# Kernel optimization log

Measured on AMD Instinct MI355X. Metric: run time of the kernel, lower is better.

## Reference

```python
import jax, jax.numpy as jnp
import numpy as np

HID, NH, QLR, KVLR, QK, VH, RH = 7168, 128, 1536, 512, 128, 128, 64
EPS = 1.1920929e-07  # torch.finfo(float32).eps, RMSNorm eps=None default
ROPE_BASE = 10000.0


def _rmsnorm(x, w):
    return x * jax.lax.rsqrt(jnp.mean(x * x, axis=-1, keepdims=True) + EPS) * w


def _rope_tables(seq_len, dim):
    inv_freq = 1.0 / (ROPE_BASE ** (np.arange(0, dim, 2, dtype=np.float32) / dim))
    t = np.arange(seq_len, dtype=np.float32)
    freqs = np.outer(t, inv_freq)          # [S, dim/2]
    emb = np.concatenate([freqs, freqs], -1)  # [S, dim]
    return jnp.asarray(np.cos(emb)), jnp.asarray(np.sin(emb))


def _apply_rope(x, cos, sin):
    # x: [B, H, S, D]; rotate-half convention matching the torch module
    d = x.shape[-1]
    x1, x2 = x[..., : d // 2], x[..., d // 2 :]
    rotated = jnp.concatenate([-x2, x1], axis=-1)
    return x * cos + rotated * sin


def setup_inputs() -> dict:
    key = jax.random.key(0)
    ks = jax.random.split(key, 9)
    def w(k, out_dim, in_dim):
        return jax.random.normal(k, (out_dim, in_dim), jnp.float32) / np.sqrt(in_dim)
    return {
        "hidden_states": jax.random.normal(ks[0], (1, 1024, HID), jnp.float32),
        "w_q_down": w(ks[1], QLR, HID),
        "q_norm_w": jnp.ones((QLR,), jnp.float32),
        "w_q_up": w(ks[2], NH * (QK + RH), QLR),
        "w_kv_down": w(ks[3], KVLR + RH, HID),
        "kv_norm_w": jnp.ones((KVLR,), jnp.float32),
        "w_kv_up": w(ks[4], NH * (QK + VH), KVLR),
        "w_out": w(ks[5], HID, NH * VH),
    }


def reference(hidden_states, w_q_down, q_norm_w, w_q_up, w_kv_down, kv_norm_w, w_kv_up, w_out):
    B, S, _ = hidden_states.shape
    cos, sin = _rope_tables(S, RH)

    # Q path: down -> RMSNorm -> up, split into non-rope / rope parts
    c_q = jnp.einsum("bsh,qh->bsq", hidden_states, w_q_down)            # [B,S,QLR]
    q_cr = jnp.einsum("bsq,oq->bso", _rmsnorm(c_q, q_norm_w), w_q_up)   # [B,S,NH*(QK+RH)]
    q_cr = q_cr.reshape(B, S, NH, QK + RH).transpose(0, 2, 1, 3)        # [B,NH,S,QK+RH]
    q_c, q_r = q_cr[..., :QK], q_cr[..., QK:]

    # KV path: shared latent + MQA rope key
    ckv_kr = jnp.einsum("bsh,oh->bso", hidden_states, w_kv_down)        # [B,S,KVLR+RH]
    c_kv, k_r = ckv_kr[..., :KVLR], ckv_kr[..., KVLR:]
    k_r = k_r[:, None, :, :]                                            # [B,1,S,RH]
    kv = jnp.einsum("bsq,oq->bso", _rmsnorm(c_kv, kv_norm_w), w_kv_up)  # [B,S,NH*(QK+VH)]
    kv = kv.reshape(B, S, NH, QK + VH).transpose(0, 2, 1, 3)            # [B,NH,S,QK+VH]
    k_c, v = kv[..., :QK], kv[..., QK:]

    q_r = _apply_rope(q_r, cos, sin)
    k_r = _apply_rope(k_r, cos, sin)

    q = jnp.concatenate([q_c, q_r], axis=-1)                            # [B,NH,S,QK+RH]
    k = jnp.concatenate([k_c, jnp.broadcast_to(k_r, (B, NH, S, RH))], axis=-1)

    scale = 1.0 / np.sqrt(QK + RH)
    scores = jnp.einsum("bhqd,bhkd->bhqk", q, k) * scale
    attn = jax.nn.softmax(scores, axis=-1)
    o = jnp.einsum("bhqk,bhkd->bhqd", attn, v)                          # [B,NH,S,VH]
    o = o.transpose(0, 2, 1, 3).reshape(B, S, NH * VH)
    return jnp.einsum("bso,ho->bsh", o, w_out)
```

## Files before the change

### kernel.cpp

```cpp
#include <hip/hip_runtime.h>
#include <hip/hip_bf16.h>
#include <math.h>

#define HIDN 7168
#define NHEAD 128
#define QLRANK 1536
#define KVLRANK 512
#define QKD 128
#define VHD 128
#define RHD 64
#define SEQ 1024
#define RMS_EPS 1.1920929e-07f

typedef unsigned short u16;
typedef __attribute__((ext_vector_type(8))) short bf16x8;
typedef __attribute__((ext_vector_type(4))) float f32x4;
typedef __attribute__((ext_vector_type(8))) unsigned short u16x8;

__device__ __forceinline__ u16 f2bf(float f) {
    unsigned int u = __float_as_uint(f);
    unsigned int r = (u + 0x7FFFu + ((u >> 16) & 1u)) >> 16;
    return (u16)r;
}
__device__ __forceinline__ float bf2f(u16 v) {
    return __uint_as_float(((unsigned int)v) << 16);
}

__device__ __forceinline__ void gld_lds16(const u16* g, u16* l) {
    __builtin_amdgcn_global_load_lds(
        (const __attribute__((address_space(1))) unsigned int*)g,
        (__attribute__((address_space(3))) unsigned int*)l,
        16, 0, 0);
}

__global__ __launch_bounds__(256) void conv3(const float* __restrict__ s0, u16* __restrict__ d0, long n0,
                                             const float* __restrict__ s1, u16* __restrict__ d1, long n1,
                                             const float* __restrict__ s2, u16* __restrict__ d2, long n2) {
    const long stride = (long)gridDim.x * blockDim.x * 8;
#pragma unroll 1
    for (int seg = 0; seg < 3; ++seg) {
        const float* s = seg == 0 ? s0 : (seg == 1 ? s1 : s2);
        u16* d        = seg == 0 ? d0 : (seg == 1 ? d1 : d2);
        long n        = seg == 0 ? n0 : (seg == 1 ? n1 : n2);
        for (long i = ((long)blockIdx.x * blockDim.x + threadIdx.x) * 8; i < n; i += stride) {
            float4 a = *(const float4*)(s + i);
            float4 b = *(const float4*)(s + i + 4);
            u16x8 o;
            o[0] = f2bf(a.x); o[1] = f2bf(a.y); o[2] = f2bf(a.z); o[3] = f2bf(a.w);
            o[4] = f2bf(b.x); o[5] = f2bf(b.y); o[6] = f2bf(b.z); o[7] = f2bf(b.w);
            *(u16x8*)(d + i) = o;
        }
    }
}

__global__ __launch_bounds__(256) void f32_to_bf16(const float* __restrict__ in,
                                                   u16* __restrict__ out, long n) {
    long i = ((long)blockIdx.x * blockDim.x + threadIdx.x) * 8;
    long stride = (long)gridDim.x * blockDim.x * 8;
    for (; i < n; i += stride) {
        float4 a = *(const float4*)(in + i);
        float4 b = *(const float4*)(in + i + 4);
        u16x8 o;
        o[0] = f2bf(a.x); o[1] = f2bf(a.y); o[2] = f2bf(a.z); o[3] = f2bf(a.w);
        o[4] = f2bf(b.x); o[5] = f2bf(b.y); o[6] = f2bf(b.z); o[7] = f2bf(b.w);
        *(u16x8*)(out + i) = o;
    }
}

template <int OUT_BF16, int FCONV>
__global__ __launch_bounds__(512) void gemm_bt(const u16* __restrict__ A,
                                               const u16* __restrict__ B,
                                               void* __restrict__ Cv,
                                               int M, int N, int Kslice, long ldk,
                                               const float* __restrict__ cvsrc,
                                               u16* __restrict__ cvdst,
                                               long cvtotal) {
    __shared__ u16 As[2 * 128 * 64];
    __shared__ u16 Bs[2 * 128 * 64];
    const int tid = threadIdx.x;
    const int lane = tid & 63;
    const int w = tid >> 6;
    const int wr = w >> 2, wc = w & 3;
    const int l15 = lane & 15, lg = lane >> 4;
    const int n0 = blockIdx.x * 128;
    const int m0 = blockIdx.y * 128;
    const long kbase = (long)blockIdx.z * Kslice;

    const u16* asrc[2];
    const u16* bsrc[2];
    int aoff[2];
#pragma unroll
    for (int i = 0; i < 2; ++i) {
        int r = (w * 2 + i) * 8 + (lane >> 3);
        int gc = (lane & 7) ^ (r & 7);
        asrc[i] = A + (long)(m0 + r) * ldk + kbase + gc * 8;
        int br = n0 + r; if (br >= N) br = N - 1;
        bsrc[i] = B + (long)br * ldk + kbase + gc * 8;
        aoff[i] = (w * 2 + i) * 512;
    }

    long gbase = 0, gend = 0;
    int nwin = 0;
    float4 cva, cvb;
    long gprev = -1;
    if (FCONV) {
        const int nblocks = gridDim.x * gridDim.y * gridDim.z;
        const int bl = (blockIdx.z * gridDim.y + blockIdx.y) * gridDim.x + blockIdx.x;
        long share = (cvtotal + nblocks - 1) / nblocks;
        gbase = (long)bl * share;
        gend = gbase + share; if (gend > cvtotal) gend = cvtotal;
        nwin = (int)((share + 511) >> 9);
    }

    f32x4 acc[4][2];
    const f32x4 z = {0.f, 0.f, 0.f, 0.f};
#pragma unroll
    for (int i = 0; i < 4; ++i)
#pragma unroll
        for (int j = 0; j < 2; ++j) acc[i][j] = z;

    auto stage = [&](int bufi, int kofs) {
#pragma unroll
        for (int i = 0; i < 2; ++i) {
            gld_lds16(asrc[i] + kofs, As + bufi * 8192 + aoff[i]);
            gld_lds16(bsrc[i] + kofs, Bs + bufi * 8192 + aoff[i]);
        }
    };

    const int nsteps = Kslice >> 6;
    stage(0, 0);
    asm volatile("s_waitcnt vmcnt(0)" ::: "memory");
    __builtin_amdgcn_s_barrier();

    int cur = 0;
    for (int t = 0; t < nsteps; ++t) {
        if (t + 1 < nsteps) stage(cur ^ 1, (t + 1) * 64);
        if (FCONV) {
            if (gprev >= 0) {
                u16x8 o;
                o[0] = f2bf(cva.x); o[1] = f2bf(cva.y); o[2] = f2bf(cva.z); o[3] = f2bf(cva.w);
                o[4] = f2bf(cvb.x); o[5] = f2bf(cvb.y); o[6] = f2bf(cvb.z); o[7] = f2bf(cvb.w);
                *(u16x8*)(cvdst + gprev * 8) = o;
            }
            gprev = -1;
            if (t < nwin) {
                long g = gbase + (long)t * 512 + tid;
                if (g < gend) {
                    cva = *(const float4*)(cvsrc + g * 8);
                    cvb = *(const float4*)(cvsrc + g * 8 + 4);
                    gprev = g;
                }
            }
        }
        const u16* Ab = As + cur * 8192;
        const u16* Bb = Bs + cur * 8192;
#pragma unroll
        for (int kk = 0; kk < 2; ++kk) {
            bf16x8 a[4], b[2];
#pragma unroll
            for (int i = 0; i < 4; ++i) {
                int row = wr * 64 + i * 16 + l15;
                a[i] = *(const bf16x8*)&Ab[row * 64 + ((kk * 4 + lg) ^ (row & 7)) * 8];
            }
#pragma unroll
            for (int j = 0; j < 2; ++j) {
                int row = wc * 32 + j * 16 + l15;
                b[j] = *(const bf16x8*)&Bb[row * 64 + ((kk * 4 + lg) ^ (row & 7)) * 8];
            }
#pragma unroll
            for (int i = 0; i < 4; ++i)
#pragma unroll
                for (int j = 0; j < 2; ++j)
                    acc[i][j] = __builtin_amdgcn_mfma_f32_16x16x32_bf16(a[i], b[j], acc[i][j], 0, 0, 0);
        }
        asm volatile("s_waitcnt vmcnt(0)" ::: "memory");
        __builtin_amdgcn_s_barrier();
        cur ^= 1;
    }
    if (FCONV && gprev >= 0) {
        u16x8 o;
        o[0] = f2bf(cva.x); o[1] = f2bf(cva.y); o[2] = f2bf(cva.z); o[3] = f2bf(cva.w);
        o[4] = f2bf(cvb.x); o[5] = f2bf(cvb.y); o[6] = f2bf(cvb.z); o[7] = f2bf(cvb.w);
        *(u16x8*)(cvdst + gprev * 8) = o;
    }

#pragma unroll
    for (int i = 0; i < 4; ++i)
#pragma unroll
        for (int j = 0; j < 2; ++j)
#pragma unroll
            for (int r = 0; r < 4; ++r) {
                int m = m0 + wr * 64 + i * 16 + lg * 4 + r;
                int n = n0 + wc * 32 + j * 16 + l15;
                if (n < N) {
                    if (OUT_BF16)
                        ((u16*)Cv)[(long)m * N + n] = f2bf(acc[i][j][r]);
                    else
                        ((float*)Cv)[(long)blockIdx.z * M * N + (long)m * N + n] = acc[i][j][r];
                }
            }
}

__global__ __launch_bounds__(256) void reduce_rms_cq(const float* __restrict__ parts,
                                                     const float* __restrict__ wnorm,
                                                     u16* __restrict__ y) {
    const int row = blockIdx.x;
    const long mn = (long)SEQ * QLRANK;
    const float* base = parts + (long)row * QLRANK;
    float v[6];
    float ss = 0.f;
#pragma unroll
    for (int i = 0; i < 6; ++i) {
        int col = i * 256 + threadIdx.x;
        float s = base[col];
#pragma unroll
        for (int p = 1; p < 4; ++p) s += base[(long)p * mn + col];
        v[i] = s;
        ss += s * s;
    }
#pragma unroll
    for (int off = 32; off > 0; off >>= 1) ss += __shfl_down(ss, off);
    __shared__ float partial[4];
    if ((threadIdx.x & 63) == 0) partial[threadIdx.x >> 6] = ss;
    __syncthreads();
    float tot = partial[0] + partial[1] + partial[2] + partial[3];
    float rs = 1.0f / sqrtf(tot / (float)QLRANK + RMS_EPS);
    u16* yr = y + (long)row * QLRANK;
#pragma unroll
    for (int i = 0; i < 6; ++i) {
        int col = i * 256 + threadIdx.x;
        yr[col] = f2bf(v[i] * rs * wnorm[col]);
    }
}

__global__ __launch_bounds__(256) void reduce_rms_rope_kv(const float* __restrict__ parts,
                                                          const float* __restrict__ wnorm,
                                                          u16* __restrict__ y,
                                                          const float* __restrict__ cos_t,
                                                          const float* __restrict__ sin_t,
                                                          u16* __restrict__ kr) {
    const int row = blockIdx.x;
    const long mn = (long)SEQ * 576;
    const float* base = parts + (long)row * 576;
    __shared__ float rope_buf[64];
    __shared__ float partial[4];
    float v[3];
    float ss = 0.f;
#pragma unroll
    for (int i = 0; i < 3; ++i) {
        int col = i * 256 + threadIdx.x;
        if (col < 576) {
            float s = base[col];
#pragma unroll
            for (int p = 1; p < 8; ++p) s += base[(long)p * mn + col];
            v[i] = s;
            if (col < KVLRANK) ss += s * s;
            else rope_buf[col - KVLRANK] = s;
        }
    }
#pragma unroll
    for (int off = 32; off > 0; off >>= 1) ss += __shfl_down(ss, off);
    if ((threadIdx.x & 63) == 0) partial[threadIdx.x >> 6] = ss;
    __syncthreads();
    float tot = partial[0] + partial[1] + partial[2] + partial[3];
    float rs = 1.0f / sqrtf(tot / (float)KVLRANK + RMS_EPS);
    u16* yr = y + (long)row * KVLRANK;
#pragma unroll
    for (int i = 0; i < 3; ++i) {
        int col = i * 256 + threadIdx.x;
        if (col < KVLRANK) yr[col] = f2bf(v[i] * rs * wnorm[col]);
    }
    if (threadIdx.x < 32) {
        float x1 = rope_buf[threadIdx.x];
        float x2 = rope_buf[threadIdx.x + 32];
        float c = cos_t[row * 32 + threadIdx.x], sn = sin_t[row * 32 + threadIdx.x];
        kr[row * 64 + threadIdx.x]      = f2bf(x1 * c - x2 * sn);
        kr[row * 64 + threadIdx.x + 32] = f2bf(x2 * c + x1 * sn);
    }
}

__global__ void rope_tables(float* __restrict__ cos_t, float* __restrict__ sin_t) {
    int s = blockIdx.x;
    int i = threadIdx.x;
    float invf = powf(10000.0f, -((float)(2 * i) / 64.0f));
    float ang = (float)s * invf;
    cos_t[s * 32 + i] = cosf(ang);
    sin_t[s * 32 + i] = sinf(ang);
}

__global__ void rope_q(u16* __restrict__ q_cr, const float* __restrict__ cos_t,
                       const float* __restrict__ sin_t) {
    int s = blockIdx.x;
    int h = blockIdx.y * 2 + (threadIdx.x >> 5);
    int i = threadIdx.x & 31;
    u16* base = q_cr + (s * (NHEAD * 192) + h * 192 + QKD);
    float x1 = bf2f(base[i]);
    float x2 = bf2f(base[i + 32]);
    float c = cos_t[s * 32 + i], sn = sin_t[s * 32 + i];
    base[i]      = f2bf(x1 * c - x2 * sn);
    base[i + 32] = f2bf(x2 * c + x1 * sn);
}

__global__ __launch_bounds__(256) void build_vt(const u16* __restrict__ kv,
                                                u16* __restrict__ vT) {
    __shared__ u16 vtile[64][136];
    const int h = blockIdx.x, sb = blockIdx.y, s0 = sb * 64;
    const int tid = threadIdx.x;
#pragma unroll
    for (int it = 0; it < 4; ++it) {
        int c = it * 256 + tid;
        int row = c >> 4;
        int off8 = (c & 15) * 8;
        *(u16x8*)&vtile[row][off8] =
            *(const u16x8*)&kv[(s0 + row) * 32768 + h * 256 + 128 + off8];
    }
    __syncthreads();
    const int sl = tid & 63;
    const int dvb = tid >> 6;
#pragma unroll
    for (int it = 0; it < 32; ++it) {
        int dv = dvb + it * 4;
        vT[(h * 128 + dv) * 1024 + s0 + sl] = vtile[sl][dv];
    }
}

__global__ __launch_bounds__(512) void mla_attn(const u16* __restrict__ q_cr,
                                                const u16* __restrict__ kv,
                                                const u16* __restrict__ kr,
                                                const u16* __restrict__ vT,
                                                u16* __restrict__ o_g,
                                                const float* __restrict__ wsrc,
                                                u16* __restrict__ wdst,
                                                int do_conv) {
    __shared__ u16 ks[64][200];
    __shared__ u16 vts[128][72];
    __shared__ u16 p_lds[8][16][68];
    const int qb = blockIdx.x, h = blockIdx.y;
    const int s0q = qb * 128;
    const int tid = threadIdx.x, lane = tid & 63, w = tid >> 6;
    const int l15 = lane & 15, lg = lane >> 4;
    const float scale = 0.07216878364870323f;

    bf16x8 qreg[6];
    {
        const int qrow = s0q + w * 16 + l15;
#pragma unroll
        for (int kk = 0; kk < 6; ++kk)
            qreg[kk] = *(const bf16x8*)&q_cr[qrow * (NHEAD * 192) + h * 192 + kk * 32 + lg * 8];
    }

    const int krow0 = tid >> 4,           koff0 = (tid & 15) * 8;
    const int krow1 = (512 + tid) >> 4,   koff1 = ((512 + tid) & 15) * 8;
    const int rrow  = tid >> 3,           roff  = (tid & 7) * 8;
    const int vdv0  = tid >> 3,           voff0 = (tid & 7) * 8;
    const int vdv1  = (512 + tid) >> 3,   voff1 = ((512 + tid) & 7) * 8;
    const u16* kvp = kv + h * 256;
    const u16* vtp = vT + (long)(h * 128) * 1024;

    u16x8 kreg0, kreg1, krreg, vreg0, vreg1;
    auto load_tile = [&](int s0k) {
        kreg0 = *(const u16x8*)&kvp[(long)(s0k + krow0) * 32768 + koff0];
        kreg1 = *(const u16x8*)&kvp[(long)(s0k + krow1) * 32768 + koff1];
        krreg = *(const u16x8*)&kr[(s0k + rrow) * 64 + roff];
        vreg0 = *(const u16x8*)&vtp[(long)vdv0 * 1024 + s0k + voff0];
        vreg1 = *(const u16x8*)&vtp[(long)vdv1 * 1024 + s0k + voff1];
    };

    const long cbase = ((long)(h * 8 + qb)) * 16 * 896;
    float4 cva0, cvb0, cva1, cvb1;
    const int gi0 = tid;
    const int gi1 = 512 + tid;
    auto conv_load = [&](int kt) {
        long g0 = cbase + (long)kt * 896;
        long a0 = (g0 + gi0) * 8;
        cva0 = *(const float4*)(wsrc + a0);
        cvb0 = *(const float4*)(wsrc + a0 + 4);
        if (gi1 < 896) {
            long a1 = (g0 + gi1) * 8;
            cva1 = *(const float4*)(wsrc + a1);
            cvb1 = *(const float4*)(wsrc + a1 + 4);
        }
    };
    auto conv_store = [&](int kt) {
        long g0 = cbase + (long)kt * 896;
        u16x8 o;
        o[0] = f2bf(cva0.x); o[1] = f2bf(cva0.y); o[2] = f2bf(cva0.z); o[3] = f2bf(cva0.w);
        o[4] = f2bf(cvb0.x); o[5] = f2bf(cvb0.y); o[6] = f2bf(cvb0.z); o[7] = f2bf(cvb0.w);
        *(u16x8*)(wdst + (g0 + gi0) * 8) = o;
        if (gi1 < 896) {
            u16x8 o1;
            o1[0] = f2bf(cva1.x); o1[1] = f2bf(cva1.y); o1[2] = f2bf(cva1.z); o1[3] = f2bf(cva1.w);
            o1[4] = f2bf(cvb1.x); o1[5] = f2bf(cvb1.y); o1[6] = f2bf(cvb1.z); o1[7] = f2bf(cvb1.w);
            *(u16x8*)(wdst + (g0 + gi1) * 8) = o1;
        }
    };

    f32x4 o_acc[8];
    const f32x4 z = {0.f, 0.f, 0.f, 0.f};
#pragma unroll
    for (int d = 0; d < 8; ++d) o_acc[d] = z;
    float m_r[4], l_r[4];
#pragma unroll
    for (int r = 0; r < 4; ++r) { m_r[r] = -1e30f; l_r[r] = 0.f; }

    load_tile(0);
    if (do_conv) conv_load(0);

    for (int kt = 0; kt < 16; ++kt) {
        __syncthreads();
        *(u16x8*)&ks[krow0][koff0]      = kreg0;
        *(u16x8*)&ks[krow1][koff1]      = kreg1;
        *(u16x8*)&ks[rrow][128 + roff]  = krreg;
        *(u16x8*)&vts[vdv0][voff0]      = vreg0;
        *(u16x8*)&vts[vdv1][voff1]      = vreg1;
        __syncthreads();
        if (kt + 1 < 16) load_tile((kt + 1) * 64);

        if (do_conv) {
            conv_store(kt);
            if (kt + 1 < 16) conv_load(kt + 1);
        }

        f32x4 sf[4];
#pragma unroll
        for (int j = 0; j < 4; ++j) sf[j] = z;
        __builtin_amdgcn_s_setprio(1);
#pragma unroll
        for (int kk = 0; kk < 6; ++kk) {
            bf16x8 a = qreg[kk];
#pragma unroll
            for (int j = 0; j < 4; ++j) {
                bf16x8 b = *(const bf16x8*)&ks[j * 16 + l15][kk * 32 + lg * 8];
                sf[j] = __builtin_amdgcn_mfma_f32_16x16x32_bf16(a, b, sf[j], 0, 0, 0);
            }
        }
        __builtin_amdgcn_s_setprio(0);

        float p[4][4];
        float alpha[4];
#pragma unroll
        for (int r = 0; r < 4; ++r) {
            float mx = fmaxf(fmaxf(sf[0][r], sf[1][r]), fmaxf(sf[2][r], sf[3][r]));
#pragma unroll
            for (int off = 1; off < 16; off <<= 1) mx = fmaxf(mx, __shfl_xor(mx, off));
            mx *= scale;
            float mnew = fmaxf(m_r[r], mx);
            alpha[r] = __expf(m_r[r] - mnew);
            float rs = 0.f;
#pragma unroll
            for (int j = 0; j < 4; ++j) {
                float pv = __expf(sf[j][r] * scale - mnew);
                p[j][r] = pv;
                rs += pv;
            }
#pragma unroll
            for (int off = 1; off < 16; off <<= 1) rs += __shfl_xor(rs, off);
            l_r[r] = l_r[r] * alpha[r] + rs;
            m_r[r] = mnew;
        }
#pragma unroll
        for (int d = 0; d < 8; ++d)
#pragma unroll
            for (int r = 0; r < 4; ++r) o_acc[d][r] *= alpha[r];

#pragma unroll
        for (int j = 0; j < 4; ++j)
#pragma unroll
            for (int r = 0; r < 4; ++r)
                p_lds[w][lg * 4 + r][j * 16 + l15] = f2bf(p[j][r]);

        __builtin_amdgcn_s_setprio(1);
#pragma unroll
        for (int kk2 = 0; kk2 < 2; ++kk2) {
            bf16x8 a = *(const bf16x8*)&p_lds[w][l15][kk2 * 32 + lg * 8];
#pragma unroll
            for (int d = 0; d < 8; ++d) {
                bf16x8 b = *(const bf16x8*)&vts[d * 16 + l15][kk2 * 32 + lg * 8];
                o_acc[d] = __builtin_amdgcn_mfma_f32_16x16x32_bf16(a, b, o_acc[d], 0, 0, 0);
            }
        }
        __builtin_amdgcn_s_setprio(0);
    }

#pragma unroll
    for (int d = 0; d < 8; ++d)
#pragma unroll
        for (int r = 0; r < 4; ++r) {
            int srow = s0q + w * 16 + lg * 4 + r;
            float v = o_acc[d][r] / l_r[r];
            o_g[srow * 16384 + h * 128 + d * 16 + l15] = f2bf(v);
        }
}

extern "C" void kernel_launch(void* const* d_in, const int* in_sizes, int n_in,
                              void* d_out, int out_size, void* d_ws, size_t ws_size,
                              hipStream_t stream) {
    const float* hs        = (const float*)d_in[0];
    const float* w_q_down  = (const float*)d_in[1];
    const float* q_norm_w  = (const float*)d_in[2];
    const float* w_q_up    = (const float*)d_in[3];
    const float* w_kv_down = (const float*)d_in[4];
    const float* kv_norm_w = (const float*)d_in[5];
    const float* w_kv_up   = (const float*)d_in[6];
    const float* w_out     = (const float*)d_in[7];
    float* out = (float*)d_out;
    char* ws = (char*)d_ws;

    const size_t SZ_KV   = (size_t)SEQ * 32768 * 2;
    const size_t SZ_QCR  = (size_t)SEQ * (NHEAD * 192) * 2;
    const size_t SZ_KR   = (size_t)SEQ * 64 * 2;
    const size_t SZ_TAB  = (size_t)SEQ * 32 * 4;
    const size_t SZ_VT   = (size_t)NHEAD * 128 * 1024 * 2;
    const size_t SZ_OG   = (size_t)SEQ * 16384 * 2;
    const size_t SZ_WOUT = (size_t)HIDN * 16384 * 2;
    const size_t SZ_WQD  = (size_t)QLRANK * HIDN * 2;
    const size_t SZ_WQU  = (size_t)24576 * QLRANK * 2;
    const size_t SZ_WKD  = (size_t)576 * HIDN * 2;
    const size_t SZ_WKU  = (size_t)32768 * KVLRANK * 2;
    const size_t SZ_PART = (size_t)4 * SEQ * QLRANK * 4;
    const size_t SZ_HS   = (size_t)SEQ * HIDN * 2;
    const size_t SZ_CQN  = (size_t)SEQ * QLRANK * 2;
    const size_t SZ_CKVN = (size_t)SEQ * KVLRANK * 2;

    size_t off = 0;
    u16* kvb     = (u16*)(ws + off); off += SZ_KV;
    u16* q_cr    = (u16*)(ws + off); off += SZ_QCR;
    u16* kr      = (u16*)(ws + off); off += SZ_KR;
    float* cos_t = (float*)(ws + off); off += SZ_TAB;
    float* sin_t = (float*)(ws + off); off += SZ_TAB;
    u16* vT      = (u16*)(ws + off); off += SZ_VT;
    u16* o_g     = (u16*)(ws + off); off += SZ_OG;
    const size_t live_end = off;
    u16* wout_bf = (u16*)(ws + live_end);
    size_t toff = live_end;
    u16* wqd_bf  = (u16*)(ws + toff); toff += SZ_WQD;
    u16* wqu_bf  = (u16*)(ws + toff); toff += SZ_WQU;
    u16* wkd_bf  = (u16*)(ws + toff); toff += SZ_WKD;
    u16* wku_bf  = (u16*)(ws + toff); toff += SZ_WKU;
    float* parts = (float*)(ws + toff); toff += SZ_PART;
    u16* hs_bf    = (u16*)(ws + toff); toff += SZ_HS;
    u16* cq_n     = (u16*)(ws + toff); toff += SZ_CQN;
    u16* ckv_n    = (u16*)(ws + toff); toff += SZ_CKVN;
    const int fuse = (live_end + SZ_WOUT) <= ws_size;
    (void)in_sizes; (void)n_in; (void)out_size;

    rope_tables<<<dim3(SEQ), dim3(32), 0, stream>>>(cos_t, sin_t);

    conv3<<<2048, 256, 0, stream>>>(hs, hs_bf, (long)SEQ * HIDN,
                                    w_q_down, wqd_bf, (long)QLRANK * HIDN,
                                    w_kv_down, wkd_bf, (long)576 * HIDN);

    gemm_bt<0, 1><<<dim3(QLRANK / 128, SEQ / 128, 4), 512, 0, stream>>>(
        hs_bf, wqd_bf, parts, SEQ, QLRANK, HIDN / 4, HIDN,
        w_q_up, wqu_bf, ((long)24576 * QLRANK) / 8);
    reduce_rms_cq<<<SEQ, 256, 0, stream>>>(parts, q_norm_w, cq_n);

    gemm_bt<1, 1><<<dim3(24576 / 128, SEQ / 128), 512, 0, stream>>>(
        cq_n, wqu_bf, q_cr, SEQ, 24576, QLRANK, QLRANK,
        w_kv_up, wku_bf, ((long)32768 * KVLRANK) / 8);

    gemm_bt<0, 0><<<dim3(5, SEQ / 128, 8), 512, 0, stream>>>(
        hs_bf, wkd_bf, parts, SEQ, 576, HIDN / 8, HIDN, nullptr, nullptr, 0);
    reduce_rms_rope_kv<<<SEQ, 256, 0, stream>>>(parts, kv_norm_w, ckv_n, cos_t, sin_t, kr);

    gemm_bt<1, 0><<<dim3(32768 / 128, SEQ / 128), 512, 0, stream>>>(
        ckv_n, wku_bf, kvb, SEQ, 32768, KVLRANK, KVLRANK, nullptr, nullptr, 0);

    rope_q<<<dim3(SEQ, NHEAD / 2), 64, 0, stream>>>(q_cr, cos_t, sin_t);
    build_vt<<<dim3(NHEAD, SEQ / 64), 256, 0, stream>>>(kvb, vT);

    if (!fuse)
        f32_to_bf16<<<4096, 256, 0, stream>>>(w_out, wout_bf, (long)HIDN * 16384);
    mla_attn<<<dim3(SEQ / 128, NHEAD), 512, 0, stream>>>(q_cr, kvb, kr, vT, o_g,
                                                         w_out, wout_bf, fuse ? 1 : 0);

    gemm_bt<0, 0><<<dim3(HIDN / 128, SEQ / 128), 512, 0, stream>>>(
        o_g, wout_bf, out, SEQ, HIDN, 16384, 16384, nullptr, nullptr, 0);
}
```

Before: 886.8 us.

## Fuse rope tables, q-rope and kv_down conversion into neighboring kernels

Merges the rope table generation into the conversion kernel and moves conversion of w_kv_down from the front conversion pass into the spare-slot conversion of the first down-projection GEMM. It also applies the Q rope rotation inside the attention kernel on the registers holding Q, which removes the separate rope_q launch and its read-modify-write of q_cr. The aim is fewer launches and less standalone memory traffic. The cost is extra branching in the GEMM conversion path and a few extra table loads per attention block.

```diff
diff --git a/kernel.cpp b/kernel.cpp
--- a/kernel.cpp
+++ b/kernel.cpp
@@ -33,15 +33,22 @@
         16, 0, 0);
 }
 
-__global__ __launch_bounds__(256) void conv3(const float* __restrict__ s0, u16* __restrict__ d0, long n0,
-                                             const float* __restrict__ s1, u16* __restrict__ d1, long n1,
-                                             const float* __restrict__ s2, u16* __restrict__ d2, long n2) {
+__global__ __launch_bounds__(256) void conv2_tab(const float* __restrict__ s0, u16* __restrict__ d0, long n0,
+                                                 const float* __restrict__ s1, u16* __restrict__ d1, long n1,
+                                                 float* __restrict__ cos_t, float* __restrict__ sin_t) {
+    if (blockIdx.x < SEQ && threadIdx.x < 32) {
+        int s = blockIdx.x, i = threadIdx.x;
+        float invf = powf(10000.0f, -((float)(2 * i) / 64.0f));
+        float ang = (float)s * invf;
+        cos_t[s * 32 + i] = cosf(ang);
+        sin_t[s * 32 + i] = sinf(ang);
+    }
     const long stride = (long)gridDim.x * blockDim.x * 8;
 #pragma unroll 1
-    for (int seg = 0; seg < 3; ++seg) {
-        const float* s = seg == 0 ? s0 : (seg == 1 ? s1 : s2);
-        u16* d        = seg == 0 ? d0 : (seg == 1 ? d1 : d2);
-        long n        = seg == 0 ? n0 : (seg == 1 ? n1 : n2);
+    for (int seg = 0; seg < 2; ++seg) {
+        const float* s = seg == 0 ? s0 : s1;
+        u16* d        = seg == 0 ? d0 : d1;
+        long n        = seg == 0 ? n0 : n1;
         for (long i = ((long)blockIdx.x * blockDim.x + threadIdx.x) * 8; i < n; i += stride) {
             float4 a = *(const float4*)(s + i);
             float4 b = *(const float4*)(s + i + 4);
@@ -72,9 +79,10 @@
                                                const u16* __restrict__ B,
                                                void* __restrict__ Cv,
                                                int M, int N, int Kslice, long ldk,
-                                               const float* __restrict__ cvsrc,
-                                               u16* __restrict__ cvdst,
-                                               long cvtotal) {
+                                               const float* __restrict__ cvs1,
+                                               u16* __restrict__ cvd1, long cvt1,
+                                               const float* __restrict__ cvs2,
+                                               u16* __restrict__ cvd2, long cvt2) {
     __shared__ u16 As[2 * 128 * 64];
     __shared__ u16 Bs[2 * 128 * 64];
     const int tid = threadIdx.x;
@@ -106,9 +114,10 @@
     if (FCONV) {
         const int nblocks = gridDim.x * gridDim.y * gridDim.z;
         const int bl = (blockIdx.z * gridDim.y + blockIdx.y) * gridDim.x + blockIdx.x;
-        long share = (cvtotal + nblocks - 1) / nblocks;
+        long total = cvt1 + cvt2;
+        long share = (total + nblocks - 1) / nblocks;
         gbase = (long)bl * share;
-        gend = gbase + share; if (gend > cvtotal) gend = cvtotal;
+        gend = gbase + share; if (gend > total) gend = total;
         nwin = (int)((share + 511) >> 9);
     }
 
@@ -140,14 +149,16 @@
                 u16x8 o;
                 o[0] = f2bf(cva.x); o[1] = f2bf(cva.y); o[2] = f2bf(cva.z); o[3] = f2bf(cva.w);
                 o[4] = f2bf(cvb.x); o[5] = f2bf(cvb.y); o[6] = f2bf(cvb.z); o[7] = f2bf(cvb.w);
-                *(u16x8*)(cvdst + gprev * 8) = o;
+                if (gprev < cvt1) *(u16x8*)(cvd1 + gprev * 8) = o;
+                else              *(u16x8*)(cvd2 + (gprev - cvt1) * 8) = o;
             }
             gprev = -1;
             if (t < nwin) {
                 long g = gbase + (long)t * 512 + tid;
                 if (g < gend) {
-                    cva = *(const float4*)(cvsrc + g * 8);
-                    cvb = *(const float4*)(cvsrc + g * 8 + 4);
+                    const float* src = (g < cvt1) ? (cvs1 + g * 8) : (cvs2 + (g - cvt1) * 8);
+                    cva = *(const float4*)(src);
+                    cvb = *(const float4*)(src + 4);
                     gprev = g;
                 }
             }
@@ -181,7 +192,8 @@
         u16x8 o;
         o[0] = f2bf(cva.x); o[1] = f2bf(cva.y); o[2] = f2bf(cva.z); o[3] = f2bf(cva.w);
         o[4] = f2bf(cvb.x); o[5] = f2bf(cvb.y); o[6] = f2bf(cvb.z); o[7] = f2bf(cvb.w);
-        *(u16x8*)(cvdst + gprev * 8) = o;
+        if (gprev < cvt1) *(u16x8*)(cvd1 + gprev * 8) = o;
+        else              *(u16x8*)(cvd2 + (gprev - cvt1) * 8) = o;
     }
 
 #pragma unroll
@@ -279,28 +291,6 @@
     }
 }
 
-__global__ void rope_tables(float* __restrict__ cos_t, float* __restrict__ sin_t) {
-    int s = blockIdx.x;
-    int i = threadIdx.x;
-    float invf = powf(10000.0f, -((float)(2 * i) / 64.0f));
-    float ang = (float)s * invf;
-    cos_t[s * 32 + i] = cosf(ang);
-    sin_t[s * 32 + i] = sinf(ang);
-}
-
-__global__ void rope_q(u16* __restrict__ q_cr, const float* __restrict__ cos_t,
-                       const float* __restrict__ sin_t) {
-    int s = blockIdx.x;
-    int h = blockIdx.y * 2 + (threadIdx.x >> 5);
-    int i = threadIdx.x & 31;
-    u16* base = q_cr + (s * (NHEAD * 192) + h * 192 + QKD);
-    float x1 = bf2f(base[i]);
-    float x2 = bf2f(base[i + 32]);
-    float c = cos_t[s * 32 + i], sn = sin_t[s * 32 + i];
-    base[i]      = f2bf(x1 * c - x2 * sn);
-    base[i + 32] = f2bf(x2 * c + x1 * sn);
-}
-
 __global__ __launch_bounds__(256) void build_vt(const u16* __restrict__ kv,
                                                 u16* __restrict__ vT) {
     __shared__ u16 vtile[64][136];
@@ -329,6 +319,8 @@
                                                 const u16* __restrict__ kr,
                                                 const u16* __restrict__ vT,
                                                 u16* __restrict__ o_g,
+                                                const float* __restrict__ cos_t,
+                                                const float* __restrict__ sin_t,
                                                 const float* __restrict__ wsrc,
                                                 u16* __restrict__ wdst,
                                                 int do_conv) {
@@ -347,6 +339,15 @@
 #pragma unroll
         for (int kk = 0; kk < 6; ++kk)
             qreg[kk] = *(const bf16x8*)&q_cr[qrow * (NHEAD * 192) + h * 192 + kk * 32 + lg * 8];
+#pragma unroll
+        for (int j = 0; j < 8; ++j) {
+            int i = lg * 8 + j;
+            float c = cos_t[qrow * 32 + i], sn = sin_t[qrow * 32 + i];
+            float x1 = bf2f((u16)qreg[4][j]);
+            float x2 = bf2f((u16)qreg[5][j]);
+            qreg[4][j] = (short)f2bf(x1 * c - x2 * sn);
+            qreg[5][j] = (short)f2bf(x2 * c + x1 * sn);
+        }
     }
 
     const int krow0 = tid >> 4,           koff0 = (tid & 15) * 8;
@@ -544,36 +545,39 @@
     const int fuse = (live_end + SZ_WOUT) <= ws_size;
     (void)in_sizes; (void)n_in; (void)out_size;
 
-    rope_tables<<<dim3(SEQ), dim3(32), 0, stream>>>(cos_t, sin_t);
-
-    conv3<<<2048, 256, 0, stream>>>(hs, hs_bf, (long)SEQ * HIDN,
-                                    w_q_down, wqd_bf, (long)QLRANK * HIDN,
-                                    w_kv_down, wkd_bf, (long)576 * HIDN);
+    conv2_tab<<<2048, 256, 0, stream>>>(hs, hs_bf, (long)SEQ * HIDN,
+                                        w_q_down, wqd_bf, (long)QLRANK * HIDN,
+                                        cos_t, sin_t);
 
     gemm_bt<0, 1><<<dim3(QLRANK / 128, SEQ / 128, 4), 512, 0, stream>>>(
         hs_bf, wqd_bf, parts, SEQ, QLRANK, HIDN / 4, HIDN,
-        w_q_up, wqu_bf, ((long)24576 * QLRANK) / 8);
+        w_q_up, wqu_bf, ((long)24576 * QLRANK) / 8,
+        w_kv_down, wkd_bf, ((long)576 * HIDN) / 8);
     reduce_rms_cq<<<SEQ, 256, 0, stream>>>(parts, q_norm_w, cq_n);
 
     gemm_bt<1, 1><<<dim3(24576 / 128, SEQ / 128), 512, 0, stream>>>(
         cq_n, wqu_bf, q_cr, SEQ, 24576, QLRANK, QLRANK,
-        w_kv_up, wku_bf, ((long)32768 * KVLRANK) / 8);
+        w_kv_up, wku_bf, ((long)32768 * KVLRANK) / 8,
+        nullptr, nullptr, 0);
 
     gemm_bt<0, 0><<<dim3(5, SEQ / 128, 8), 512, 0, stream>>>(
-        hs_bf, wkd_bf, parts, SEQ, 576, HIDN / 8, HIDN, nullptr, nullptr, 0);
+        hs_bf, wkd_bf, parts, SEQ, 576, HIDN / 8, HIDN,
+        nullptr, nullptr, 0, nullptr, nullptr, 0);
     reduce_rms_rope_kv<<<SEQ, 256, 0, stream>>>(parts, kv_norm_w, ckv_n, cos_t, sin_t, kr);
 
     gemm_bt<1, 0><<<dim3(32768 / 128, SEQ / 128), 512, 0, stream>>>(
-        ckv_n, wku_bf, kvb, SEQ, 32768, KVLRANK, KVLRANK, nullptr, nullptr, 0);
-
-    rope_q<<<dim3(SEQ, NHEAD / 2), 64, 0, stream>>>(q_cr, cos_t, sin_t);
+        ckv_n, wku_bf, kvb, SEQ, 32768, KVLRANK, KVLRANK,
+        nullptr, nullptr, 0, nullptr, nullptr, 0);
+
     build_vt<<<dim3(NHEAD, SEQ / 64), 256, 0, stream>>>(kvb, vT);
 
     if (!fuse)
         f32_to_bf16<<<4096, 256, 0, stream>>>(w_out, wout_bf, (long)HIDN * 16384);
     mla_attn<<<dim3(SEQ / 128, NHEAD), 512, 0, stream>>>(q_cr, kvb, kr, vT, o_g,
+                                                         cos_t, sin_t,
                                                          w_out, wout_bf, fuse ? 1 : 0);
 
     gemm_bt<0, 0><<<dim3(HIDN / 128, SEQ / 128), 512, 0, stream>>>(
-        o_g, wout_bf, out, SEQ, HIDN, 16384, 16384, nullptr, nullptr, 0);
-}
+        o_g, wout_bf, out, SEQ, HIDN, 16384, 16384,
+        nullptr, nullptr, 0, nullptr, nullptr, 0);
+}
```

After: 866.5 us. -2.3%, faster.
